# Performance work log

Measured on AMD Instinct MI355X. Metric: run time of the kernel, lower is better.

## Reference

```python
import jax, jax.numpy as jnp
import numpy as np

N = 50000
E = 1600000
IN_C = 512
HID = 64
OUT_C = 64
HEADS = 2
K = 2
NEG_SLOPE = 0.2


def setup_inputs() -> dict:
    key = jax.random.key(0)
    ks = jax.random.split(key, 9)
    x = jax.random.normal(ks[0], (N, IN_C), dtype=jnp.float32)
    edge_index = jax.random.randint(ks[1], (2, E), 0, N, dtype=jnp.int64)
    edge_attr = jax.random.uniform(ks[2], (E,), dtype=jnp.float32)
    # SGConv linear (glorot-ish init)
    W_sg = jax.random.normal(ks[3], (IN_C, HID), dtype=jnp.float32) / np.sqrt(IN_C)
    b_sg = jnp.zeros((HID,), dtype=jnp.float32)
    # GATConv: lin (no bias), attention vectors, output bias (concat=False -> size OUT_C)
    W_gat = jax.random.normal(ks[4], (HID, HEADS * OUT_C), dtype=jnp.float32) / np.sqrt(HID)
    att_src = jax.random.normal(ks[5], (HEADS, OUT_C), dtype=jnp.float32) / np.sqrt(OUT_C)
    att_dst = jax.random.normal(ks[6], (HEADS, OUT_C), dtype=jnp.float32) / np.sqrt(OUT_C)
    b_gat = jnp.zeros((OUT_C,), dtype=jnp.float32)
    return {"x": x, "edge_index": edge_index, "edge_attr": edge_attr,
            "W_sg": W_sg, "b_sg": b_sg, "W_gat": W_gat,
            "att_src": att_src, "att_dst": att_dst, "b_gat": b_gat}


def reference(x, edge_index, edge_attr, W_sg, b_sg, W_gat, att_src, att_dst, b_gat):
    n = x.shape[0]
    src, dst = edge_index[0], edge_index[1]
    # add self-loops (weight 1) once; reused by SGConv (gcn_norm) and GAT
    loop = jnp.arange(n, dtype=src.dtype)
    src2 = jnp.concatenate([src, loop])
    dst2 = jnp.concatenate([dst, loop])
    ew = jnp.concatenate([edge_attr, jnp.ones((n,), x.dtype)])

    # ---- SGConv: K hops of D^-1/2 A D^-1/2, then linear ----
    deg = jax.ops.segment_sum(ew, dst2, num_segments=n)
    dinv = jnp.where(deg > 0, jax.lax.rsqrt(deg), 0.0)
    norm = dinv[src2] * ew * dinv[dst2]  # [E+N]
    h = x
    for _ in range(K):
        h = jax.ops.segment_sum(norm[:, None] * h[src2], dst2, num_segments=n)
    h = h @ W_sg + b_sg  # [N, HID]

    # activation (SELU); dropout is identity in eval mode
    h = jax.nn.selu(h)

    # ---- GATConv (heads, concat=False -> mean over heads) ----
    g = (h @ W_gat).reshape(n, HEADS, OUT_C)  # [N, H, C]
    a_src = jnp.einsum('nhc,hc->nh', g, att_src)  # [N, H]
    a_dst = jnp.einsum('nhc,hc->nh', g, att_dst)
    e = jax.nn.leaky_relu(a_src[src2] + a_dst[dst2], NEG_SLOPE)  # [E+N, H]
    # per-destination softmax (numerically stable)
    emax = jax.ops.segment_max(e, dst2, num_segments=n)
    emax = jnp.where(jnp.isfinite(emax), emax, 0.0)
    ee = jnp.exp(e - emax[dst2])
    denom = jax.ops.segment_sum(ee, dst2, num_segments=n)
    alpha = ee / jnp.maximum(denom[dst2], 1e-16)  # [E+N, H]
    out = jax.ops.segment_sum(alpha[:, :, None] * g[src2], dst2, num_segments=n)  # [N, H, C]
    return out.mean(axis=1) + b_gat  # [N, OUT_C]
```

## Files before the change

kernel.cpp:

```cpp
#include <hip/hip_runtime.h>
#include <hip/hip_fp16.h>
#include <math.h>

#define N_NODES 50000
#define N_EDGES 1600000
#define IN_CH 512
#define HID 64
#define OUTC 64
#define NEG_SLOPE 0.2f
#define EA_SCALE 131072.0f
#define PCAP 128

typedef __attribute__((ext_vector_type(8))) short bf16x8;
typedef __attribute__((ext_vector_type(4))) float f32x4;

__device__ __forceinline__ unsigned bf16r(float f) {
    unsigned b = __float_as_uint(f);
    return (b + 0x7FFFu + ((b >> 16) & 1u)) >> 16;
}

__global__ void k_wsplit(const float* __restrict__ W, short* __restrict__ Wfrag) {
    int idx = blockIdx.x * 256 + threadIdx.x;
    if (idx >= IN_CH * HID) return;
    int k = idx >> 6, c = idx & 63;
    float wv = W[idx];
    unsigned h = bf16r(wv);
    float res = wv - __uint_as_float(h << 16);
    unsigned l = bf16r(res);
    int kstep = k >> 5, cb = c >> 4;
    int lane = (c & 15) | (((k >> 3) & 3) << 4);
    int j = k & 7;
    int base = ((kstep * 4 + cb) * 2) * 512 + lane * 8 + j;
    Wfrag[base] = (short)h;
    Wfrag[base + 512] = (short)l;
}

#define G1R 64
#define G1KC 64
__global__ __launch_bounds__(256) void k_gemm_hist(const float* __restrict__ x,
                                                   const short* __restrict__ Wfrag,
                                                   __half* __restrict__ p,
                                                   const int* __restrict__ dst,
                                                   const float* __restrict__ ea,
                                                   unsigned* __restrict__ deg32,
                                                   unsigned short* __restrict__ rank) {
    __shared__ float xs[G1R][G1KC + 4];
    int tid = threadIdx.x;
    int bid = blockIdx.x;

    if (bid & 1) {
        int e0 = (bid >> 1) * 2048;
        int e1 = e0 + 2048; if (e1 > N_EDGES) e1 = N_EDGES;
        for (int e = e0 + tid; e < e1; e += 256) {
            int d = dst[e];
            unsigned pack = (1u << 24) | (unsigned)(ea[e] * EA_SCALE);
            unsigned old = atomicAdd(&deg32[d], pack);
            rank[e] = (unsigned short)(old >> 24);
        }
        return;
    }

    int lane = tid & 63, wv = tid >> 6;
    int r0 = (bid >> 1) * G1R;
    f32x4 acc0 = {0.f, 0.f, 0.f, 0.f};
    f32x4 acc1 = {0.f, 0.f, 0.f, 0.f};
    f32x4 acc2 = {0.f, 0.f, 0.f, 0.f};
    f32x4 acc3 = {0.f, 0.f, 0.f, 0.f};

    for (int k0 = 0; k0 < IN_CH; k0 += G1KC) {
#pragma unroll
        for (int it = 0; it < 4; it++) {
            int row = it * 16 + (tid >> 4);
            int gr = r0 + row;
            float4 v = make_float4(0.f, 0.f, 0.f, 0.f);
            if (gr < N_NODES)
                v = *(const float4*)(x + (size_t)gr * IN_CH + k0 + (tid & 15) * 4);
            *(float4*)&xs[row][(tid & 15) * 4] = v;
        }
        __syncthreads();
#pragma unroll
        for (int kk = 0; kk < 2; kk++) {
            int ks = (k0 >> 5) + kk;
            const short* wb = Wfrag + ks * 4096 + (lane << 3);
            bf16x8 bh0 = *(const bf16x8*)(wb);
            bf16x8 bl0 = *(const bf16x8*)(wb + 512);
            bf16x8 bh1 = *(const bf16x8*)(wb + 1024);
            bf16x8 bl1 = *(const bf16x8*)(wb + 1536);
            bf16x8 bh2 = *(const bf16x8*)(wb + 2048);
            bf16x8 bl2 = *(const bf16x8*)(wb + 2560);
            bf16x8 bh3 = *(const bf16x8*)(wb + 3072);
            bf16x8 bl3 = *(const bf16x8*)(wb + 3584);
            int arow = wv * 16 + (lane & 15);
            int acol = kk * 32 + ((lane >> 4) << 3);
            float4 xa = *(const float4*)&xs[arow][acol];
            float4 xb = *(const float4*)&xs[arow][acol + 4];
            float xv[8] = {xa.x, xa.y, xa.z, xa.w, xb.x, xb.y, xb.z, xb.w};
            bf16x8 ah, al;
#pragma unroll
            for (int j = 0; j < 8; j++) {
                unsigned b = __float_as_uint(xv[j]);
                float res = xv[j] - __uint_as_float(b & 0xFFFF0000u);
                ah[j] = (short)(b >> 16);
                al[j] = (short)(__float_as_uint(res) >> 16);
            }
            acc0 = __builtin_amdgcn_mfma_f32_16x16x32_bf16(ah, bh0, acc0, 0, 0, 0);
            acc0 = __builtin_amdgcn_mfma_f32_16x16x32_bf16(ah, bl0, acc0, 0, 0, 0);
            acc0 = __builtin_amdgcn_mfma_f32_16x16x32_bf16(al, bh0, acc0, 0, 0, 0);
            acc1 = __builtin_amdgcn_mfma_f32_16x16x32_bf16(ah, bh1, acc1, 0, 0, 0);
            acc1 = __builtin_amdgcn_mfma_f32_16x16x32_bf16(ah, bl1, acc1, 0, 0, 0);
            acc1 = __builtin_amdgcn_mfma_f32_16x16x32_bf16(al, bh1, acc1, 0, 0, 0);
            acc2 = __builtin_amdgcn_mfma_f32_16x16x32_bf16(ah, bh2, acc2, 0, 0, 0);
            acc2 = __builtin_amdgcn_mfma_f32_16x16x32_bf16(ah, bl2, acc2, 0, 0, 0);
            acc2 = __builtin_amdgcn_mfma_f32_16x16x32_bf16(al, bh2, acc2, 0, 0, 0);
            acc3 = __builtin_amdgcn_mfma_f32_16x16x32_bf16(ah, bh3, acc3, 0, 0, 0);
            acc3 = __builtin_amdgcn_mfma_f32_16x16x32_bf16(ah, bl3, acc3, 0, 0, 0);
            acc3 = __builtin_amdgcn_mfma_f32_16x16x32_bf16(al, bh3, acc3, 0, 0, 0);
        }
        __syncthreads();
    }
    int crow = r0 + wv * 16 + ((lane >> 4) << 2);
    int ccol = lane & 15;
#pragma unroll
    for (int r = 0; r < 4; r++) {
        int gr = crow + r;
        if (gr < N_NODES) {
            p[(unsigned)gr * HID + ccol]      = __float2half(acc0[r]);
            p[(unsigned)gr * HID + 16 + ccol] = __float2half(acc1[r]);
            p[(unsigned)gr * HID + 32 + ccol] = __float2half(acc2[r]);
            p[(unsigned)gr * HID + 48 + ccol] = __float2half(acc3[r]);
        }
    }
}

__global__ void k_scan_reduce(const unsigned* __restrict__ deg32,
                              int* bsum, float* dinv, int n) {
    __shared__ int lds[256];
    int i = blockIdx.x * 256 + threadIdx.x;
    unsigned dv = (i < n) ? deg32[i] : 0u;
    lds[threadIdx.x] = (int)(dv >> 24);
    if (i < n)
        dinv[i] = rsqrtf(1.0f + (float)(dv & 0xFFFFFFu) * (1.0f / EA_SCALE));
    __syncthreads();
    for (int s = 128; s > 0; s >>= 1) {
        if (threadIdx.x < s) lds[threadIdx.x] += lds[threadIdx.x + s];
        __syncthreads();
    }
    if (threadIdx.x == 0) bsum[blockIdx.x] = lds[0];
}

__global__ void k_scan_bsum(int* bsum, int nb) {
    __shared__ int lds[256];
    int t = threadIdx.x;
    int v = (t < nb) ? bsum[t] : 0;
    lds[t] = v;
    __syncthreads();
    for (int s = 1; s < 256; s <<= 1) {
        int add = (t >= s) ? lds[t - s] : 0;
        __syncthreads();
        lds[t] += add;
        __syncthreads();
    }
    if (t < nb) bsum[t] = lds[t] - v;
}

__global__ void k_scan_final(const unsigned* __restrict__ deg32,
                             const int* __restrict__ bsum,
                             int* offsets, int n) {
    __shared__ int lds[256];
    int t = threadIdx.x;
    int i = blockIdx.x * 256 + t;
    int v = (i < n) ? (int)(deg32[i] >> 24) : 0;
    lds[t] = v;
    __syncthreads();
    for (int s = 1; s < 256; s <<= 1) {
        int add = (t >= s) ? lds[t - s] : 0;
        __syncthreads();
        lds[t] += add;
        __syncthreads();
    }
    int incl = lds[t];
    int base = bsum[blockIdx.x];
    if (i < n) offsets[i] = base + incl - v;
    if (i == n - 1) offsets[n] = base + incl;
}

__global__ void k_scatter(const int* __restrict__ src, const int* __restrict__ dst,
                          const float* __restrict__ ea, const float* __restrict__ dinv,
                          const int* __restrict__ offsets,
                          const unsigned short* __restrict__ rank,
                          int2* __restrict__ edges) {
    int e = blockIdx.x * blockDim.x + threadIdx.x;
    if (e >= N_EDGES) return;
    int s = src[e], d = dst[e];
    int pos = offsets[d] + rank[e];
    edges[pos] = make_int2(s << 5, __float_as_int(dinv[s] * ea[e] * dinv[d]));
}

__global__ __launch_bounds__(256) void k_hop(const unsigned* __restrict__ hin2,
                                             const int* __restrict__ offsets,
                                             const int2* __restrict__ edges,
                                             const float* __restrict__ dinv,
                                             unsigned* __restrict__ hout2) {
    __shared__ float2 part[2][32];
    int tid = threadIdx.x;
    int w = tid >> 6, lane = tid & 63;
    int slot = w >> 1, half = w & 1;
    int cl = lane & 31, es = lane >> 5;
    int v = blockIdx.x * 2 + slot;
    int beg = offsets[v], end = offsets[v + 1];
    int mid = beg + ((end - beg) >> 1);
    int lo = half ? mid : beg;
    int hi = half ? end : mid;
    float ax = 0.f, ay = 0.f, bx = 0.f, by = 0.f;
    float cx = 0.f, cy = 0.f, dx = 0.f, dy = 0.f;
    if (!half && !es) {
        float dv = dinv[v];
        float sw = dv * dv;
        unsigned gh = hin2[(unsigned)v * 32 + cl];
        float2 hf = __half22float2(*(__half2*)&gh);
        ax = sw * hf.x; ay = sw * hf.y;
    }
    int i = lo;
    for (; i + 8 <= hi; i += 8) {
        int2 e0 = edges[i + es];
        int2 e1 = edges[i + 2 + es];
        int2 e2 = edges[i + 4 + es];
        int2 e3 = edges[i + 6 + es];
        unsigned g0 = hin2[(unsigned)(e0.x + cl)];
        unsigned g1 = hin2[(unsigned)(e1.x + cl)];
        unsigned g2 = hin2[(unsigned)(e2.x + cl)];
        unsigned g3 = hin2[(unsigned)(e3.x + cl)];
        float w0 = __int_as_float(e0.y), w1 = __int_as_float(e1.y);
        float w2 = __int_as_float(e2.y), w3 = __int_as_float(e3.y);
        float2 h0 = __half22float2(*(__half2*)&g0);
        float2 h1 = __half22float2(*(__half2*)&g1);
        float2 h2 = __half22float2(*(__half2*)&g2);
        float2 h3 = __half22float2(*(__half2*)&g3);
        ax += w0 * h0.x; ay += w0 * h0.y;
        bx += w1 * h1.x; by += w1 * h1.y;
        cx += w2 * h2.x; cy += w2 * h2.y;
        dx += w3 * h3.x; dy += w3 * h3.y;
    }
    for (; i + es < hi; i += 2) {
        int2 e0 = edges[i + es];
        unsigned g0 = hin2[(unsigned)(e0.x + cl)];
        float w0 = __int_as_float(e0.y);
        float2 h0 = __half22float2(*(__half2*)&g0);
        ax += w0 * h0.x; ay += w0 * h0.y;
    }
    ax += bx + cx + dx; ay += by + cy + dy;
    ax += __shfl_xor(ax, 32);
    ay += __shfl_xor(ay, 32);
    if (half && lane < 32) part[slot][cl] = make_float2(ax, ay);
    __syncthreads();
    if (!half && lane < 32) {
        float2 pp = part[slot][cl];
        __half2 hp = __floats2half2_rn(ax + pp.x, ay + pp.y);
        hout2[(unsigned)v * 32 + cl] = *(unsigned*)&hp;
    }
}

#define G2_ROWS 32
__global__ __launch_bounds__(256) void k_act_gemm2(const __half* __restrict__ h2,
                                                   const float* __restrict__ bsg,
                                                   const float* __restrict__ Wg,
                                                   const float* __restrict__ att_s,
                                                   const float* __restrict__ att_d,
                                                   uint2* __restrict__ g4h,
                                                   float2* __restrict__ asrc2,
                                                   float4* __restrict__ admm) {
    __shared__ float hs[G2_ROWS][HID];
    int tid = threadIdx.x;
    int wave = tid >> 6, lane = tid & 63;
    int r0 = blockIdx.x * G2_ROWS;
    int rbase = wave * 8;

    const float SC = 1.0507009873554805f, AL = 1.6732632423543772f;
    {
        int row = tid >> 3, c0 = (tid & 7) * 8;
        int r = r0 + row;
        float vals[8];
        if (r < N_NODES) {
            uint4 raw = *(const uint4*)(h2 + (unsigned)r * HID + c0);
            float2 f0 = __half22float2(*(__half2*)&raw.x);
            float2 f1 = __half22float2(*(__half2*)&raw.y);
            float2 f2 = __half22float2(*(__half2*)&raw.z);
            float2 f3 = __half22float2(*(__half2*)&raw.w);
            vals[0] = f0.x; vals[1] = f0.y; vals[2] = f1.x; vals[3] = f1.y;
            vals[4] = f2.x; vals[5] = f2.y; vals[6] = f3.x; vals[7] = f3.y;
        } else {
#pragma unroll
            for (int j = 0; j < 8; j++) vals[j] = 0.f;
        }
#pragma unroll
        for (int j = 0; j < 8; j++) {
            float hv = vals[j] + bsg[c0 + j];
            hv = (hv > 0.f) ? SC * hv : SC * AL * (__expf(hv) - 1.f);
            hs[row][c0 + j] = hv;
        }
    }
    __syncthreads();

    float accx[8], accy[8];
#pragma unroll
    for (int j = 0; j < 8; j++) { accx[j] = 0.f; accy[j] = 0.f; }
#pragma unroll 2
    for (int k = 0; k < HID; k++) {
        float w0 = Wg[(size_t)k * 128 + lane];
        float w1 = Wg[(size_t)k * 128 + 64 + lane];
#pragma unroll
        for (int j = 0; j < 8; j++) {
            float hk = hs[rbase + j][k];
            accx[j] += hk * w0;
            accy[j] += hk * w1;
        }
    }
    float ats0 = att_s[lane], ats1 = att_s[64 + lane];
    float atd0 = att_d[lane], atd1 = att_d[64 + lane];
#pragma unroll
    for (int j = 0; j < 8; j++) {
        int v = r0 + rbase + j;
        if (v >= N_NODES) break;
        __half2 gp = __floats2half2_rn(accx[j], accy[j]);
        unsigned gpu = *(unsigned*)&gp;
        unsigned other = (unsigned)__shfl_xor((int)gpu, 1);
        if (!(lane & 1)) g4h[(unsigned)v * 32 + (lane >> 1)] = make_uint2(gpu, other);
        float s0 = accx[j] * ats0, s1 = accy[j] * ats1;
        float d0 = accx[j] * atd0, d1 = accy[j] * atd1;
#pragma unroll
        for (int o = 32; o > 0; o >>= 1) {
            s0 += __shfl_xor(s0, o);
            s1 += __shfl_xor(s1, o);
            d0 += __shfl_xor(d0, o);
            d1 += __shfl_xor(d1, o);
        }
        if (lane == 0) {
            asrc2[v] = make_float2(s0, s1);
            float m0 = s0 + d0; m0 = (m0 > 0.f) ? m0 : NEG_SLOPE * m0;
            float m1 = s1 + d1; m1 = (m1 > 0.f) ? m1 : NEG_SLOPE * m1;
            admm[v] = make_float4(d0, d1, m0, m1);
        }
    }
}

__global__ __launch_bounds__(256) void k_gat(const uint2* __restrict__ g4h,
                                             const float2* __restrict__ asrc2,
                                             const float4* __restrict__ admm,
                                             const int* __restrict__ offsets,
                                             const int2* __restrict__ edges,
                                             const float* __restrict__ bgat,
                                             float* __restrict__ out) {
    __shared__ int4 pbuf[2][2][PCAP];
    __shared__ float4 pacc[2][32];
    __shared__ float2 pden[2][32];
    int tid = threadIdx.x;
    int w = tid >> 6, lane = tid & 63;
    int slot = w >> 1, half = w & 1;
    int cl = lane & 31, es = lane >> 5;
    int v = blockIdx.x * 2 + slot;
    float4 am = admm[v];
    int beg = offsets[v], end = offsets[v + 1];
    int mid = beg + ((end - beg) >> 1);
    int lo = half ? mid : beg;
    int hi = half ? end : mid;
    int n = hi - lo;

    float pd0 = 0.f, pd1 = 0.f;
    for (int i = lo + lane; i < hi; i += 64) {
        int2 e = edges[i];
        float2 a = asrc2[(unsigned)e.x >> 5];
        float t0 = a.x + am.x; t0 = (t0 > 0.f) ? t0 : NEG_SLOPE * t0;
        float t1 = a.y + am.y; t1 = (t1 > 0.f) ? t1 : NEG_SLOPE * t1;
        float p0 = __expf(t0 - am.z);
        float p1 = __expf(t1 - am.w);
        int idx = i - lo;
        if (idx < PCAP)
            pbuf[slot][half][idx] = make_int4(e.x, __float_as_int(p0), __float_as_int(p1), 0);
        pd0 += p0; pd1 += p1;
    }
#pragma unroll
    for (int o = 32; o > 0; o >>= 1) {
        pd0 += __shfl_xor(pd0, o);
        pd1 += __shfl_xor(pd1, o);
    }
    if (!half) { pd0 += 1.f; pd1 += 1.f; }

    float aA = 0.f, aB = 0.f, aC = 0.f, aD = 0.f;
    float bA = 0.f, bB = 0.f, bC = 0.f, bD = 0.f;
    if (!half && !es) {
        uint2 gs = g4h[(unsigned)v * 32 + cl];
        float2 gx = __half22float2(*(__half2*)&gs.x);
        float2 gy = __half22float2(*(__half2*)&gs.y);
        aA = gx.x; aB = gx.y; aC = gy.x; aD = gy.y;
    }
    int n1 = (n < PCAP) ? n : PCAP;
    int ii = 0;
    for (; ii + 8 <= n1; ii += 8) {
        int4 e0 = pbuf[slot][half][ii + es];
        int4 e1 = pbuf[slot][half][ii + 2 + es];
        int4 e2 = pbuf[slot][half][ii + 4 + es];
        int4 e3 = pbuf[slot][half][ii + 6 + es];
        uint2 g0 = g4h[(unsigned)(e0.x + cl)];
        uint2 g1 = g4h[(unsigned)(e1.x + cl)];
        uint2 g2 = g4h[(unsigned)(e2.x + cl)];
        uint2 g3 = g4h[(unsigned)(e3.x + cl)];
        float p00 = __int_as_float(e0.y), p01 = __int_as_float(e0.z);
        float p10 = __int_as_float(e1.y), p11 = __int_as_float(e1.z);
        float p20 = __int_as_float(e2.y), p21 = __int_as_float(e2.z);
        float p30 = __int_as_float(e3.y), p31 = __int_as_float(e3.z);
        float2 g0x = __half22float2(*(__half2*)&g0.x);
        float2 g0y = __half22float2(*(__half2*)&g0.y);
        float2 g1x = __half22float2(*(__half2*)&g1.x);
        float2 g1y = __half22float2(*(__half2*)&g1.y);
        float2 g2x = __half22float2(*(__half2*)&g2.x);
        float2 g2y = __half22float2(*(__half2*)&g2.y);
        float2 g3x = __half22float2(*(__half2*)&g3.x);
        float2 g3y = __half22float2(*(__half2*)&g3.y);
        aA += p00 * g0x.x; aB += p01 * g0x.y; aC += p00 * g0y.x; aD += p01 * g0y.y;
        bA += p10 * g1x.x; bB += p11 * g1x.y; bC += p10 * g1y.x; bD += p11 * g1y.y;
        aA += p20 * g2x.x; aB += p21 * g2x.y; aC += p20 * g2y.x; aD += p21 * g2y.y;
        bA += p30 * g3x.x; bB += p31 * g3x.y; bC += p30 * g3y.x; bD += p31 * g3y.y;
    }
    for (; ii + es < n1; ii += 2) {
        int4 e0 = pbuf[slot][half][ii + es];
        uint2 g0 = g4h[(unsigned)(e0.x + cl)];
        float p00 = __int_as_float(e0.y), p01 = __int_as_float(e0.z);
        float2 g0x = __half22float2(*(__half2*)&g0.x);
        float2 g0y = __half22float2(*(__half2*)&g0.y);
        aA += p00 * g0x.x; aB += p01 * g0x.y; aC += p00 * g0y.x; aD += p01 * g0y.y;
    }
    for (int jj = PCAP + es; jj < n; jj += 2) {
        int2 e = edges[lo + jj];
        float2 a = asrc2[(unsigned)e.x >> 5];
        float t0 = a.x + am.x; t0 = (t0 > 0.f) ? t0 : NEG_SLOPE * t0;
        float t1 = a.y + am.y; t1 = (t1 > 0.f) ? t1 : NEG_SLOPE * t1;
        float p0 = __expf(t0 - am.z);
        float p1 = __expf(t1 - am.w);
        uint2 g0 = g4h[(unsigned)(e.x + cl)];
        float2 g0x = __half22float2(*(__half2*)&g0.x);
        float2 g0y = __half22float2(*(__half2*)&g0.y);
        aA += p0 * g0x.x; aB += p1 * g0x.y; aC += p0 * g0y.x; aD += p1 * g0y.y;
    }
    aA += bA; aB += bB; aC += bC; aD += bD;
    aA += __shfl_xor(aA, 32); aB += __shfl_xor(aB, 32);
    aC += __shfl_xor(aC, 32); aD += __shfl_xor(aD, 32);
    if (half && lane < 32) {
        pacc[slot][cl] = make_float4(aA, aB, aC, aD);
        pden[slot][cl] = make_float2(pd0, pd1);
    }
    __syncthreads();
    if (!half && lane < 32) {
        float4 pa = pacc[slot][cl];
        float2 pd = pden[slot][cl];
        float r0 = 1.f / (pd0 + pd.x), r1 = 1.f / (pd1 + pd.y);
        float oe = 0.5f * ((aA + pa.x) * r0 + (aB + pa.y) * r1) + bgat[cl * 2];
        float oo = 0.5f * ((aC + pa.z) * r0 + (aD + pa.w) * r1) + bgat[cl * 2 + 1];
        *(float2*)&out[(unsigned)v * OUTC + cl * 2] = make_float2(oe, oo);
    }
}

extern "C" void kernel_launch(void* const* d_in, const int* in_sizes, int n_in,
                              void* d_out, int out_size, void* d_ws, size_t ws_size,
                              hipStream_t stream) {
    const float* x     = (const float*)d_in[0];
    const int*   ei    = (const int*)d_in[1];
    const float* ea    = (const float*)d_in[2];
    const float* Wsg   = (const float*)d_in[3];
    const float* bsg   = (const float*)d_in[4];
    const float* Wg    = (const float*)d_in[5];
    const float* att_s = (const float*)d_in[6];
    const float* att_d = (const float*)d_in[7];
    const float* bgat  = (const float*)d_in[8];
    const int* src = ei;
    const int* dst = ei + N_EDGES;
    float* out = (float*)d_out;

    char* ws = (char*)d_ws;
    size_t off = 0;
    auto alloc = [&](size_t bytes) -> void* {
        void* p = ws + off;
        off = (off + bytes + 255) & ~(size_t)255;
        return p;
    };
    unsigned*       deg32  = (unsigned*)alloc((size_t)N_NODES * 4);
    float*          dinv   = (float*)alloc((size_t)N_NODES * 4);
    unsigned short* rank   = (unsigned short*)alloc((size_t)N_EDGES * 2);
    int*            offs   = (int*)alloc((size_t)(N_NODES + 1) * 4);
    int*            bsum   = (int*)alloc(256 * 4);
    int2*           edges  = (int2*)alloc((size_t)N_EDGES * 8);
    short*          Wfrag  = (short*)alloc((size_t)IN_CH * HID * 2 * 2);
    __half*         h0     = (__half*)alloc((size_t)N_NODES * HID * 2);
    __half*         h1     = (__half*)alloc((size_t)N_NODES * HID * 2);
    uint2*          g4h    = (uint2*)alloc((size_t)N_NODES * 32 * 8);
    float2*         asrc2  = (float2*)alloc((size_t)N_NODES * 8);
    float4*         admm   = (float4*)alloc((size_t)N_NODES * 16);
    (void)ws_size; (void)in_sizes; (void)n_in; (void)out_size;

    hipMemsetAsync(deg32, 0, (size_t)N_NODES * 4, stream);

    k_wsplit<<<(IN_CH * HID + 255) / 256, 256, 0, stream>>>(Wsg, Wfrag);

    k_gemm_hist<<<1564, 256, 0, stream>>>(x, Wfrag, h0, dst, ea, deg32, rank);

    int nb = (N_NODES + 255) / 256;
    k_scan_reduce<<<nb, 256, 0, stream>>>(deg32, bsum, dinv, N_NODES);
    k_scan_bsum<<<1, 256, 0, stream>>>(bsum, nb);
    k_scan_final<<<nb, 256, 0, stream>>>(deg32, bsum, offs, N_NODES);

    k_scatter<<<(N_EDGES + 255) / 256, 256, 0, stream>>>(src, dst, ea, dinv, offs, rank, edges);

    k_hop<<<N_NODES / 2, 256, 0, stream>>>((const unsigned*)h0, offs, edges, dinv, (unsigned*)h1);
    k_hop<<<N_NODES / 2, 256, 0, stream>>>((const unsigned*)h1, offs, edges, dinv, (unsigned*)h0);
    k_act_gemm2<<<(N_NODES + G2_ROWS - 1) / G2_ROWS, 256, 0, stream>>>(h0, bsg, Wg, att_s, att_d, g4h, asrc2, admm);
    k_gat<<<N_NODES / 2, 256, 0, stream>>>(g4h, asrc2, admm, offs, edges, bgat, out);
}
```

Measured before the change: 320.4 us.

## Double-buffer x tiles via direct global-to-LDS loads with XOR swizzle

Replaces the register-staged x tile load in the first GEMM with global_load_lds DMA into a double-buffered LDS tile, prefetching the next K chunk while MFMAs run on the current one. Padding is dropped in favor of an XOR swizzle on column groups to avoid bank conflicts. Out-of-range rows are clamped instead of zeroed, and LDS usage doubles, which may reduce occupancy.

After: 320.7 us. Within noise of the previous version (+0.1%).

```diff
diff --git a/kernel.cpp b/kernel.cpp
--- a/kernel.cpp
+++ b/kernel.cpp
@@ -17,6 +17,12 @@
 __device__ __forceinline__ unsigned bf16r(float f) {
     unsigned b = __float_as_uint(f);
     return (b + 0x7FFFu + ((b >> 16) & 1u)) >> 16;
+}
+
+__device__ __forceinline__ void gload16(const void* g, void* l) {
+    __builtin_amdgcn_global_load_lds(
+        (const __attribute__((address_space(1))) void*)g,
+        (__attribute__((address_space(3))) void*)l, 16, 0, 0);
 }
 
 __global__ void k_wsplit(const float* __restrict__ W, short* __restrict__ Wfrag) {
@@ -44,7 +50,7 @@
                                                    const float* __restrict__ ea,
                                                    unsigned* __restrict__ deg32,
                                                    unsigned short* __restrict__ rank) {
-    __shared__ float xs[G1R][G1KC + 4];
+    __shared__ float xs[2][G1R][G1KC];
     int tid = threadIdx.x;
     int bid = blockIdx.x;
 
@@ -67,17 +73,26 @@
     f32x4 acc2 = {0.f, 0.f, 0.f, 0.f};
     f32x4 acc3 = {0.f, 0.f, 0.f, 0.f};
 
+    auto stage = [&](int b, int k0) {
+#pragma unroll
+        for (int it = 0; it < 4; it++) {
+            int rowbase = it * 16 + wv * 4;
+            int row = rowbase + (lane >> 4);
+            int gr = r0 + row; if (gr > N_NODES - 1) gr = N_NODES - 1;
+            int col = ((lane & 15) ^ (row & 7)) << 2;
+            gload16(x + (size_t)gr * IN_CH + k0 + col, &xs[b][rowbase][0]);
+        }
+    };
+
+    stage(0, 0);
+    asm volatile("s_waitcnt vmcnt(0)" ::: "memory");
+    __syncthreads();
+
+    int cur = 0;
+    int arow = wv * 16 + (lane & 15);
+    const char* xsbase = (const char*)&xs[0][0][0];
     for (int k0 = 0; k0 < IN_CH; k0 += G1KC) {
-#pragma unroll
-        for (int it = 0; it < 4; it++) {
-            int row = it * 16 + (tid >> 4);
-            int gr = r0 + row;
-            float4 v = make_float4(0.f, 0.f, 0.f, 0.f);
-            if (gr < N_NODES)
-                v = *(const float4*)(x + (size_t)gr * IN_CH + k0 + (tid & 15) * 4);
-            *(float4*)&xs[row][(tid & 15) * 4] = v;
-        }
-        __syncthreads();
+        if (k0 + G1KC < IN_CH) stage(cur ^ 1, k0 + G1KC);
 #pragma unroll
         for (int kk = 0; kk < 2; kk++) {
             int ks = (k0 >> 5) + kk;
@@ -90,10 +105,10 @@
             bf16x8 bl2 = *(const bf16x8*)(wb + 2560);
             bf16x8 bh3 = *(const bf16x8*)(wb + 3072);
             bf16x8 bl3 = *(const bf16x8*)(wb + 3584);
-            int arow = wv * 16 + (lane & 15);
-            int acol = kk * 32 + ((lane >> 4) << 3);
-            float4 xa = *(const float4*)&xs[arow][acol];
-            float4 xb = *(const float4*)&xs[arow][acol + 4];
+            int c16 = kk * 8 + ((lane >> 4) << 1);
+            size_t rb = (size_t)cur * (G1R * G1KC * 4) + (size_t)arow * (G1KC * 4);
+            float4 xa = *(const float4*)(xsbase + rb + (((c16    ) ^ (arow & 7)) << 4));
+            float4 xb = *(const float4*)(xsbase + rb + (((c16 + 1) ^ (arow & 7)) << 4));
             float xv[8] = {xa.x, xa.y, xa.z, xa.w, xb.x, xb.y, xb.z, xb.w};
             bf16x8 ah, al;
 #pragma unroll
@@ -116,7 +131,9 @@
             acc3 = __builtin_amdgcn_mfma_f32_16x16x32_bf16(ah, bl3, acc3, 0, 0, 0);
             acc3 = __builtin_amdgcn_mfma_f32_16x16x32_bf16(al, bh3, acc3, 0, 0, 0);
         }
+        asm volatile("s_waitcnt vmcnt(0)" ::: "memory");
         __syncthreads();
+        cur ^= 1;
     }
     int crow = r0 + wv * 16 + ((lane >> 4) << 2);
     int ccol = lane & 15;
```
